# Kernel tuning notes

Measured on AMD Instinct MI355X. Metric: run time of the kernel, lower is better.

## Reference

```python
import jax, jax.numpy as jnp
import numpy as np

B, S, D, MAX_LEN = 4, 2048, 512, 2048
V = 2 * MAX_LEN + 1  # embedding table size
POS_MAX = 3000


def setup_inputs() -> dict:
    key = jax.random.key(0)
    k1, k2, k3 = jax.random.split(key, 3)
    x = jax.random.normal(k1, (B, S, D), dtype=jnp.float32)
    emb_table = jax.random.normal(k2, (V, D), dtype=jnp.float32) * 0.02
    positions = jnp.sort(jax.random.randint(k3, (B, S), 0, POS_MAX), axis=-1)
    return {"x": x, "emb_table": emb_table, "positions": positions}


def reference(x, emb_table, positions):
    # x: [B,S,D], emb_table: [2M+1, D], positions: [B,S] int
    Bc, Sc, _ = x.shape
    Vc = emb_table.shape[0]
    M = (Vc - 1) // 2
    # rel[b,i,j] = clamp(pos_i - pos_j, -M, M) + M   -> index into table
    rel = jnp.clip(positions[:, :, None] - positions[:, None, :], -M, M) + M  # [B,S,S]
    # mean_j emb[rel[b,i,j]] == (occurrence counts over V) @ table / S
    # counts[b,i,v] = #{j : rel[b,i,j] == v}; identical math, no [B,S,S,D] tensor.
    b_idx = jnp.arange(Bc)[:, None, None]
    i_idx = jnp.arange(Sc)[None, :, None]
    counts = jnp.zeros((Bc, Sc, Vc), dtype=x.dtype).at[b_idx, i_idx, rel].add(1.0)
    mean_emb = jnp.einsum('bsv,vd->bsd', counts, emb_table) / Sc  # [B,S,D]
    return x + mean_emb
```

## Files before the change

### kernel.cpp

```cpp
#include <hip/hip_runtime.h>
#include <hip/hip_bf16.h>
#include <cstdint>

#define NB 4
#define NS 2048
#define ND 512
#define NM 2048
#define NV 4097
#define NP 3000
#define TROW 8192
#define CCC 5104
#define EVW 4128
#define RSW 3080

typedef __bf16 bf16x8 __attribute__((ext_vector_type(8)));
typedef float f32x4 __attribute__((ext_vector_type(4)));

typedef const unsigned int __attribute__((address_space(1)))* as1_u32p;
typedef unsigned int __attribute__((address_space(3)))* as3_u32p;

__device__ __forceinline__ void gll16(const void* g, void* l) {
  __builtin_amdgcn_global_load_lds((as1_u32p)g, (as3_u32p)l, 16, 0, 0);
}

__device__ __forceinline__ unsigned short f2bf(float f) {
  union { __bf16 b; unsigned short u; } cv;
  cv.b = (__bf16)f;
  return cv.u;
}

__device__ __forceinline__ int lbound_dev(const int* a, int n, int key) {
  int lo = 0, hi = n;
  while (lo < hi) { int mid = (lo + hi) >> 1; if (a[mid] < key) lo = mid + 1; else hi = mid; }
  return lo;
}

__global__ void k1_hist(const int* __restrict__ pos, unsigned int* __restrict__ hist,
                        int* __restrict__ rs) {
  __shared__ unsigned int h[NP];
  int b = blockIdx.x, tid = threadIdx.x;
  for (int i = tid; i < NP; i += 256) h[i] = 0u;
  __syncthreads();
  const int* pb = pos + b * NS;
  for (int i = tid; i < NS; i += 256) atomicAdd(&h[pb[i]], 1u);
  __syncthreads();
  unsigned int* hb = hist + b * NP;
  for (int i = tid; i < NP; i += 256) hb[i] = h[i];
  for (int t = tid; t <= 3072; t += 256) rs[b * RSW + t] = lbound_dev(pb, NS, t);
}

__global__ void k2_htrev(const unsigned int* __restrict__ hist, unsigned short* __restrict__ HT) {
  int idx = blockIdx.x * 256 + threadIdx.x;
  int b = idx >> 14, rem = idx & 16383;
  int u = rem >> 10, t8 = rem & 1023;
  const unsigned int* hb = hist + b * NP;
  int basep = CCC + u - t8 * 8;
  union { unsigned short us[8]; uint4 v4; } pk;
#pragma unroll
  for (int e = 0; e < 8; ++e) {
    int p = basep - e;
    float f = (p >= 0 && p < NP) ? (float)hb[p] : 0.0f;
    pk.us[e] = f2bf(f);
  }
  *(uint4*)(HT + (size_t)(b * 16 + u) * TROW + t8 * 8) = pk.v4;
}

__global__ void k3_ebf(const float* __restrict__ emb, unsigned short* __restrict__ EB) {
  __shared__ float tile[64][65];
  int v0 = blockIdx.x * 64, d0 = blockIdx.y * 64, tid = threadIdx.x;
  int c = tid & 63, r0 = tid >> 6;
#pragma unroll
  for (int k = 0; k < 16; ++k) {
    int r = k * 4 + r0;
    int v = v0 + r;
    float val = 0.f;
    if (v < NV && v != 0 && v != (NV - 1)) val = emb[(size_t)v * ND + d0 + c];
    tile[r][c] = val;
  }
  __syncthreads();
  int vv0 = (tid & 7) * 8;
#pragma unroll
  for (int k2 = 0; k2 < 2; ++k2) {
    int dd = (tid >> 3) + k2 * 32;
    if (v0 + vv0 + 8 <= EVW) {
      union { unsigned short us[8]; uint4 v4; } pk;
#pragma unroll
      for (int e = 0; e < 8; ++e) pk.us[e] = f2bf(tile[vv0 + e][dd]);
      *(uint4*)(EB + (size_t)(d0 + dd) * EVW + v0 + vv0) = pk.v4;
    }
  }
}

__global__ __launch_bounds__(256, 3)
void k4_gemm(const unsigned short* __restrict__ HT, const unsigned short* __restrict__ EB,
             const int* __restrict__ rs, const float* __restrict__ x,
             const float* __restrict__ emb, float* __restrict__ out) {
  int Q0 = blockIdx.x * 64, d0 = blockIdx.y * 128, b = blockIdx.z;
  int tid = threadIdx.x, w = tid >> 6, lane = tid & 63;
  int wm = w >> 1, wn = w & 1;
  __shared__ unsigned short As[2][2048];
  __shared__ unsigned short Bs[2][4096];

  const unsigned short* HTb = HT + (size_t)b * 16 * TROW;
  int ul = lane & 15, gl = lane >> 4;

  int v_lo = (Q0 > 951) ? ((Q0 - 951) & ~31) : 0;
  int v_hi = Q0 + 2112; if (v_hi > EVW) v_hi = EVW;

  f32x4 acc[2][4];
#pragma unroll
  for (int a1 = 0; a1 < 2; ++a1)
#pragma unroll
    for (int a2 = 0; a2 < 4; ++a2) { f32x4 z = {0.f, 0.f, 0.f, 0.f}; acc[a1][a2] = z; }

  const unsigned short* asrc_lane = HTb + ul * TROW + gl * 8;

  auto stage = [&](int sbuf, int kk) {
    int t0 = CCC - Q0 - NM - 16 * w + kk;
    gll16(asrc_lane + t0, &As[sbuf][w * 512]);
#pragma unroll
    for (int ci = 0; ci < 2; ++ci) {
      int c = w + ci * 4;
      const unsigned short* bsrc = EB + (size_t)(d0 + c * 16 + ul) * EVW + kk + gl * 8;
      gll16(bsrc, &Bs[sbuf][c * 512]);
    }
  };

  stage(0, v_lo);
  __syncthreads();

  int aoff = (lane >> 4) * 128 + (lane & 15) * 8;
  int buf = 0;
  for (int kk = v_lo; kk < v_hi; kk += 32) {
    if (kk + 32 < v_hi) stage(buf ^ 1, kk + 32);
    bf16x8 af[2], bfr[4];
#pragma unroll
    for (int mf = 0; mf < 2; ++mf)
      af[mf] = *reinterpret_cast<const bf16x8*>(&As[buf][(wm * 2 + mf) * 512 + aoff]);
#pragma unroll
    for (int nf = 0; nf < 4; ++nf)
      bfr[nf] = *reinterpret_cast<const bf16x8*>(&Bs[buf][(wn * 4 + nf) * 512 + aoff]);
#pragma unroll
    for (int mf = 0; mf < 2; ++mf)
#pragma unroll
      for (int nf = 0; nf < 4; ++nf)
        acc[mf][nf] = __builtin_amdgcn_mfma_f32_16x16x32_bf16(af[mf], bfr[nf], acc[mf][nf], 0, 0, 0);
    __syncthreads();
    buf ^= 1;
  }

  const int* rsb = rs + b * RSW;
  const float* xb = x + (size_t)b * NS * ND;
  float* outb = out + (size_t)b * NS * ND;
  int col = lane & 15, rb4 = (lane >> 4) * 4;
#pragma unroll
  for (int nf = 0; nf < 4; ++nf) {
    int dcol = d0 + wn * 64 + nf * 16 + col;
    float e0v = emb[dcol];
    float eMv = emb[(size_t)(NV - 1) * ND + dcol];
#pragma unroll
    for (int mf = 0; mf < 2; ++mf) {
#pragma unroll
      for (int j = 0; j < 4; ++j) {
        int q = Q0 + wm * 32 + mf * 16 + rb4 + j;
        if (q >= NP) continue;
        int i0 = rsb[q], i1 = rsb[q + 1];
        if (i0 == i1) continue;
        int cge = (q >= NM) ? rsb[q - NM + 1] : 0;
        int cle = (q + NM < NP) ? (NS - rsb[q + NM]) : 0;
        float val = (acc[mf][nf][j] + (float)cge * eMv + (float)cle * e0v) * (1.0f / (float)NS);
        for (int i = i0; i < i1; ++i)
          outb[(size_t)i * ND + dcol] = xb[(size_t)i * ND + dcol] + val;
      }
    }
  }
}

extern "C" void kernel_launch(void* const* d_in, const int* in_sizes, int n_in,
                              void* d_out, int out_size, void* d_ws, size_t ws_size,
                              hipStream_t stream) {
  const float* x = (const float*)d_in[0];
  const float* emb = (const float*)d_in[1];
  const int* pos = (const int*)d_in[2];
  float* out = (float*)d_out;

  char* ws = (char*)d_ws;
  unsigned short* HT = (unsigned short*)(ws);
  unsigned short* EB = (unsigned short*)(ws + 1048576);
  unsigned int* hist = (unsigned int*)(ws + 5275648);
  int* rs = (int*)(ws + 5323648);

  hipLaunchKernelGGL(k1_hist, dim3(NB), dim3(256), 0, stream, pos, hist, rs);
  hipLaunchKernelGGL(k2_htrev, dim3(256), dim3(256), 0, stream, hist, HT);
  hipLaunchKernelGGL(k3_ebf, dim3(65, 8), dim3(256), 0, stream, emb, EB);
  hipLaunchKernelGGL(k4_gemm, dim3(47, 4, NB), dim3(256), 0, stream, HT, EB, rs, x, emb, out);
}
```

Before: 188.2 us.

## Triple-buffer GEMM LDS pipeline with manual waitcnt and split rank-search kernel

The GEMM main loop moves from double to triple buffering of the A/B LDS tiles. It uses explicit s_waitcnt vmcnt/lgkmcnt plus a single barrier per iteration, so async global-to-LDS loads run two tiles ahead, and it raises wave priority around the MFMA block. The binary-search rank computation leaves the 4-block histogram kernel for its own wider-grid kernel, so it gets more parallelism. Occupancy hint goes from 3 to 4 blocks per CU. The trade-offs are more LDS per block, an extra kernel launch, and hand-tuned waitcnt counts that must match the number of loads issued per stage.

```diff
diff --git a/kernel.cpp b/kernel.cpp
--- a/kernel.cpp
+++ b/kernel.cpp
@@ -35,8 +35,7 @@
   return lo;
 }
 
-__global__ void k1_hist(const int* __restrict__ pos, unsigned int* __restrict__ hist,
-                        int* __restrict__ rs) {
+__global__ void k1_hist(const int* __restrict__ pos, unsigned int* __restrict__ hist) {
   __shared__ unsigned int h[NP];
   int b = blockIdx.x, tid = threadIdx.x;
   for (int i = tid; i < NP; i += 256) h[i] = 0u;
@@ -46,7 +45,13 @@
   __syncthreads();
   unsigned int* hb = hist + b * NP;
   for (int i = tid; i < NP; i += 256) hb[i] = h[i];
-  for (int t = tid; t <= 3072; t += 256) rs[b * RSW + t] = lbound_dev(pb, NS, t);
+}
+
+__global__ void k1b_rs(const int* __restrict__ pos, int* __restrict__ rs) {
+  int t = blockIdx.x * 256 + threadIdx.x;
+  int b = blockIdx.y;
+  if (t > 3072) return;
+  rs[b * RSW + t] = lbound_dev(pos + b * NS, NS, t);
 }
 
 __global__ void k2_htrev(const unsigned int* __restrict__ hist, unsigned short* __restrict__ HT) {
@@ -91,21 +96,22 @@
   }
 }
 
-__global__ __launch_bounds__(256, 3)
+__global__ __launch_bounds__(256, 4)
 void k4_gemm(const unsigned short* __restrict__ HT, const unsigned short* __restrict__ EB,
              const int* __restrict__ rs, const float* __restrict__ x,
              const float* __restrict__ emb, float* __restrict__ out) {
   int Q0 = blockIdx.x * 64, d0 = blockIdx.y * 128, b = blockIdx.z;
   int tid = threadIdx.x, w = tid >> 6, lane = tid & 63;
   int wm = w >> 1, wn = w & 1;
-  __shared__ unsigned short As[2][2048];
-  __shared__ unsigned short Bs[2][4096];
+  __shared__ unsigned short As[3][2048];
+  __shared__ unsigned short Bs[3][4096];
 
   const unsigned short* HTb = HT + (size_t)b * 16 * TROW;
   int ul = lane & 15, gl = lane >> 4;
 
   int v_lo = (Q0 > 951) ? ((Q0 - 951) & ~31) : 0;
   int v_hi = Q0 + 2112; if (v_hi > EVW) v_hi = EVW;
+  int nt = (v_hi - v_lo) >> 5;
 
   f32x4 acc[2][4];
 #pragma unroll
@@ -115,7 +121,8 @@
 
   const unsigned short* asrc_lane = HTb + ul * TROW + gl * 8;
 
-  auto stage = [&](int sbuf, int kk) {
+  auto stage = [&](int sbuf, int t) {
+    int kk = v_lo + t * 32;
     int t0 = CCC - Q0 - NM - 16 * w + kk;
     gll16(asrc_lane + t0, &As[sbuf][w * 512]);
 #pragma unroll
@@ -126,27 +133,32 @@
     }
   };
 
-  stage(0, v_lo);
-  __syncthreads();
+  stage(0, 0);
+  stage(1, 1);
 
   int aoff = (lane >> 4) * 128 + (lane & 15) * 8;
-  int buf = 0;
-  for (int kk = v_lo; kk < v_hi; kk += 32) {
-    if (kk + 32 < v_hi) stage(buf ^ 1, kk + 32);
+  int s0 = 0, s1 = 1, s2 = 2;
+  for (int t = 0; t < nt; ++t) {
+    if (t + 1 < nt) asm volatile("s_waitcnt vmcnt(3) lgkmcnt(0)" ::: "memory");
+    else            asm volatile("s_waitcnt vmcnt(0) lgkmcnt(0)" ::: "memory");
+    __builtin_amdgcn_s_barrier();
+    if (t + 2 < nt) stage(s2, t + 2);
+
     bf16x8 af[2], bfr[4];
 #pragma unroll
     for (int mf = 0; mf < 2; ++mf)
-      af[mf] = *reinterpret_cast<const bf16x8*>(&As[buf][(wm * 2 + mf) * 512 + aoff]);
+      af[mf] = *reinterpret_cast<const bf16x8*>(&As[s0][(wm * 2 + mf) * 512 + aoff]);
 #pragma unroll
     for (int nf = 0; nf < 4; ++nf)
-      bfr[nf] = *reinterpret_cast<const bf16x8*>(&Bs[buf][(wn * 4 + nf) * 512 + aoff]);
+      bfr[nf] = *reinterpret_cast<const bf16x8*>(&Bs[s0][(wn * 4 + nf) * 512 + aoff]);
+    __builtin_amdgcn_s_setprio(1);
 #pragma unroll
     for (int mf = 0; mf < 2; ++mf)
 #pragma unroll
       for (int nf = 0; nf < 4; ++nf)
         acc[mf][nf] = __builtin_amdgcn_mfma_f32_16x16x32_bf16(af[mf], bfr[nf], acc[mf][nf], 0, 0, 0);
-    __syncthreads();
-    buf ^= 1;
+    __builtin_amdgcn_s_setprio(0);
+    int tmp = s0; s0 = s1; s1 = s2; s2 = tmp;
   }
 
   const int* rsb = rs + b * RSW;
@@ -190,7 +202,8 @@
   unsigned int* hist = (unsigned int*)(ws + 5275648);
   int* rs = (int*)(ws + 5323648);
 
-  hipLaunchKernelGGL(k1_hist, dim3(NB), dim3(256), 0, stream, pos, hist, rs);
+  hipLaunchKernelGGL(k1_hist, dim3(NB), dim3(256), 0, stream, pos, hist);
+  hipLaunchKernelGGL(k1b_rs, dim3(13, NB), dim3(256), 0, stream, pos, rs);
   hipLaunchKernelGGL(k2_htrev, dim3(256), dim3(256), 0, stream, hist, HT);
   hipLaunchKernelGGL(k3_ebf, dim3(65, 8), dim3(256), 0, stream, emb, EB);
   hipLaunchKernelGGL(k4_gemm, dim3(47, 4, NB), dim3(256), 0, stream, HT, EB, rs, x, emb, out);
```

Result: faster. 178.7 us (-5.1%).

## Pre-swizzle operands into MFMA fragment layout and drop LDS staging in GEMM

Applied to the files above, without the earlier changes.

The Toeplitz histogram and the bf16 embedding table are now written in a fragment-interleaved layout, so each lane loads its MFMA operand straight from global memory with one 16-byte load. The GEMM no longer stages through LDS or calls __syncthreads. Instead each wave owns a 32x64 tile with per-wave K bounds and keeps a three-deep register prefetch. The rank-search, Toeplitz build and embedding conversion kernels are merged into one prep launch, and the k1_hist work is split so rs is computed in parallel blocks. In exchange, operands are no longer shared between waves through LDS, which means more global and L2 traffic.

```diff
diff --git a/kernel.cpp b/kernel.cpp
--- a/kernel.cpp
+++ b/kernel.cpp
@@ -8,20 +8,12 @@
 #define NM 2048
 #define NV 4097
 #define NP 3000
-#define TROW 8192
-#define CCC 5104
-#define EVW 4128
 #define RSW 3080
+#define EBI_KB 129
+#define HTI_BATCH_BYTES (2 * 256 * 1024)
 
 typedef __bf16 bf16x8 __attribute__((ext_vector_type(8)));
 typedef float f32x4 __attribute__((ext_vector_type(4)));
-
-typedef const unsigned int __attribute__((address_space(1)))* as1_u32p;
-typedef unsigned int __attribute__((address_space(3)))* as3_u32p;
-
-__device__ __forceinline__ void gll16(const void* g, void* l) {
-  __builtin_amdgcn_global_load_lds((as1_u32p)g, (as3_u32p)l, 16, 0, 0);
-}
 
 __device__ __forceinline__ unsigned short f2bf(float f) {
   union { __bf16 b; unsigned short u; } cv;
@@ -35,8 +27,7 @@
   return lo;
 }
 
-__global__ void k1_hist(const int* __restrict__ pos, unsigned int* __restrict__ hist,
-                        int* __restrict__ rs) {
+__global__ void k1_hist(const int* __restrict__ pos, unsigned int* __restrict__ hist) {
   __shared__ unsigned int h[NP];
   int b = blockIdx.x, tid = threadIdx.x;
   for (int i = tid; i < NP; i += 256) h[i] = 0u;
@@ -46,66 +37,114 @@
   __syncthreads();
   unsigned int* hb = hist + b * NP;
   for (int i = tid; i < NP; i += 256) hb[i] = h[i];
-  for (int t = tid; t <= 3072; t += 256) rs[b * RSW + t] = lbound_dev(pb, NS, t);
-}
-
-__global__ void k2_htrev(const unsigned int* __restrict__ hist, unsigned short* __restrict__ HT) {
-  int idx = blockIdx.x * 256 + threadIdx.x;
-  int b = idx >> 14, rem = idx & 16383;
-  int u = rem >> 10, t8 = rem & 1023;
-  const unsigned int* hb = hist + b * NP;
-  int basep = CCC + u - t8 * 8;
-  union { unsigned short us[8]; uint4 v4; } pk;
-#pragma unroll
-  for (int e = 0; e < 8; ++e) {
-    int p = basep - e;
-    float f = (p >= 0 && p < NP) ? (float)hb[p] : 0.0f;
-    pk.us[e] = f2bf(f);
-  }
-  *(uint4*)(HT + (size_t)(b * 16 + u) * TROW + t8 * 8) = pk.v4;
-}
-
-__global__ void k3_ebf(const float* __restrict__ emb, unsigned short* __restrict__ EB) {
+}
+
+__global__ void k_prep(const int* __restrict__ pos, const unsigned int* __restrict__ hist,
+                       const float* __restrict__ emb, unsigned short* __restrict__ HTI,
+                       unsigned short* __restrict__ EBI, int* __restrict__ rs) {
   __shared__ float tile[64][65];
-  int v0 = blockIdx.x * 64, d0 = blockIdx.y * 64, tid = threadIdx.x;
-  int c = tid & 63, r0 = tid >> 6;
-#pragma unroll
-  for (int k = 0; k < 16; ++k) {
-    int r = k * 4 + r0;
-    int v = v0 + r;
-    float val = 0.f;
-    if (v < NV && v != 0 && v != (NV - 1)) val = emb[(size_t)v * ND + d0 + c];
-    tile[r][c] = val;
-  }
-  __syncthreads();
-  int vv0 = (tid & 7) * 8;
-#pragma unroll
-  for (int k2 = 0; k2 < 2; ++k2) {
-    int dd = (tid >> 3) + k2 * 32;
-    if (v0 + vv0 + 8 <= EVW) {
-      union { unsigned short us[8]; uint4 v4; } pk;
-#pragma unroll
-      for (int e = 0; e < 8; ++e) pk.us[e] = f2bf(tile[vv0 + e][dd]);
-      *(uint4*)(EB + (size_t)(d0 + dd) * EVW + v0 + vv0) = pk.v4;
-    }
-  }
-}
-
-__global__ __launch_bounds__(256, 3)
-void k4_gemm(const unsigned short* __restrict__ HT, const unsigned short* __restrict__ EB,
+  int blk = blockIdx.x, tid = threadIdx.x;
+  if (blk < 52) {
+    int b = blk & 3, chunk = blk >> 2;
+    int t = chunk * 256 + tid;
+    if (t <= 3072) rs[b * RSW + t] = lbound_dev(pos + b * NS, NS, t);
+    return;
+  }
+  if (blk < 564) {
+    int idx = (blk - 52) * 256 + tid;
+    int l = idx & 63;
+    int tb = (idx >> 6) & 255;
+    int p = (idx >> 14) & 1;
+    int bb = idx >> 15;
+    const unsigned int* hbt = hist + bb * NP;
+    int base = 5104 + (l & 15) - tb * 32 - p * 16 - ((l >> 4) * 8);
+    union { unsigned short us[8]; uint4 v4; } pk;
+#pragma unroll
+    for (int e = 0; e < 8; ++e) {
+      int ii = base - e;
+      float f = (ii >= 0 && ii < NP) ? (float)hbt[ii] : 0.0f;
+      pk.us[e] = f2bf(f);
+    }
+    *(uint4*)(HTI + ((size_t)(bb * 2 + p) * 256 + tb) * 512 + l * 8) = pk.v4;
+    return;
+  }
+  {
+    int blk2 = blk - 564;
+    int v0 = (blk2 % 65) * 64, d0 = (blk2 / 65) * 64;
+    int c = tid & 63, r0 = tid >> 6;
+#pragma unroll
+    for (int k = 0; k < 16; ++k) {
+      int r = k * 4 + r0;
+      int v = v0 + r;
+      float val = 0.f;
+      if (v < NV && v != 0 && v != (NV - 1)) val = emb[(size_t)v * ND + d0 + c];
+      tile[r][c] = val;
+    }
+    __syncthreads();
+#pragma unroll
+    for (int rep = 0; rep < 2; ++rep) {
+      int tile_id = rep * 4 + (tid >> 6);
+      int l = tid & 63;
+      int kb_loc = tile_id >> 2, dt_loc = tile_id & 3;
+      int kb = (v0 >> 5) + kb_loc, dt = (d0 >> 4) + dt_loc;
+      if (kb < EBI_KB) {
+        union { unsigned short us[8]; uint4 v4; } pk;
+#pragma unroll
+        for (int e = 0; e < 8; ++e)
+          pk.us[e] = f2bf(tile[kb_loc * 32 + ((l >> 4) * 8) + e][dt_loc * 16 + (l & 15)]);
+        *(uint4*)(EBI + ((size_t)dt * EBI_KB + kb) * 512 + l * 8) = pk.v4;
+      }
+    }
+  }
+}
+
+#define LOADSET(sa0, sa1, sb0, sb1, sb2, sb3, tt)                                   \
+  if ((tt) < nt) {                                                                  \
+    int tof = (tt) * 1024 + vo;                                                     \
+    sa0 = *(const bf16x8*)(hb + (size_t)(cA0 + tof));                               \
+    sa1 = *(const bf16x8*)(hb + (size_t)(cA1 + tof));                               \
+    sb0 = *(const bf16x8*)(eb + (size_t)(cB0 + tof));                               \
+    sb1 = *(const bf16x8*)(eb + (size_t)(cB1 + tof));                               \
+    sb2 = *(const bf16x8*)(eb + (size_t)(cB2 + tof));                               \
+    sb3 = *(const bf16x8*)(eb + (size_t)(cB3 + tof));                               \
+  }
+
+#define MMSET(sa0, sa1, sb0, sb1, sb2, sb3)                                         \
+  acc[0][0] = __builtin_amdgcn_mfma_f32_16x16x32_bf16(sa0, sb0, acc[0][0], 0, 0, 0);\
+  acc[0][1] = __builtin_amdgcn_mfma_f32_16x16x32_bf16(sa0, sb1, acc[0][1], 0, 0, 0);\
+  acc[0][2] = __builtin_amdgcn_mfma_f32_16x16x32_bf16(sa0, sb2, acc[0][2], 0, 0, 0);\
+  acc[0][3] = __builtin_amdgcn_mfma_f32_16x16x32_bf16(sa0, sb3, acc[0][3], 0, 0, 0);\
+  acc[1][0] = __builtin_amdgcn_mfma_f32_16x16x32_bf16(sa1, sb0, acc[1][0], 0, 0, 0);\
+  acc[1][1] = __builtin_amdgcn_mfma_f32_16x16x32_bf16(sa1, sb1, acc[1][1], 0, 0, 0);\
+  acc[1][2] = __builtin_amdgcn_mfma_f32_16x16x32_bf16(sa1, sb2, acc[1][2], 0, 0, 0);\
+  acc[1][3] = __builtin_amdgcn_mfma_f32_16x16x32_bf16(sa1, sb3, acc[1][3], 0, 0, 0);
+
+__global__ __launch_bounds__(256, 4)
+void k4_gemm(const unsigned short* __restrict__ HTI, const unsigned short* __restrict__ EBI,
              const int* __restrict__ rs, const float* __restrict__ x,
              const float* __restrict__ emb, float* __restrict__ out) {
-  int Q0 = blockIdx.x * 64, d0 = blockIdx.y * 128, b = blockIdx.z;
   int tid = threadIdx.x, w = tid >> 6, lane = tid & 63;
-  int wm = w >> 1, wn = w & 1;
-  __shared__ unsigned short As[2][2048];
-  __shared__ unsigned short Bs[2][4096];
-
-  const unsigned short* HTb = HT + (size_t)b * 16 * TROW;
-  int ul = lane & 15, gl = lane >> 4;
-
-  int v_lo = (Q0 > 951) ? ((Q0 - 951) & ~31) : 0;
-  int v_hi = Q0 + 2112; if (v_hi > EVW) v_hi = EVW;
+  int b = blockIdx.z;
+  int Q0w = blockIdx.x * 128 + w * 32;
+  int D0w = blockIdx.y * 64;
+
+  int v_lo = (Q0w > 951) ? ((Q0w - 951) & ~31) : 0;
+  int v_hi = Q0w + 2080; if (v_hi > 4128) v_hi = 4128;
+  int nt = (v_hi - v_lo) >> 5;
+
+  const char* hb = (const char*)HTI + (size_t)b * HTI_BATCH_BYTES;
+  const char* eb = (const char*)EBI;
+
+  int S0 = 3056 - Q0w + v_lo;
+  int S1 = S0 - 16;
+  int cA0 = (((S0 >> 4) & 1) * 256 + (S0 >> 5)) * 1024;
+  int cA1 = (((S1 >> 4) & 1) * 256 + (S1 >> 5)) * 1024;
+  int kb0 = v_lo >> 5, dt0 = D0w >> 4;
+  int cB0 = ((dt0 + 0) * EBI_KB + kb0) * 1024;
+  int cB1 = ((dt0 + 1) * EBI_KB + kb0) * 1024;
+  int cB2 = ((dt0 + 2) * EBI_KB + kb0) * 1024;
+  int cB3 = ((dt0 + 3) * EBI_KB + kb0) * 1024;
+  int vo = lane * 16;
 
   f32x4 acc[2][4];
 #pragma unroll
@@ -113,40 +152,24 @@
 #pragma unroll
     for (int a2 = 0; a2 < 4; ++a2) { f32x4 z = {0.f, 0.f, 0.f, 0.f}; acc[a1][a2] = z; }
 
-  const unsigned short* asrc_lane = HTb + ul * TROW + gl * 8;
-
-  auto stage = [&](int sbuf, int kk) {
-    int t0 = CCC - Q0 - NM - 16 * w + kk;
-    gll16(asrc_lane + t0, &As[sbuf][w * 512]);
-#pragma unroll
-    for (int ci = 0; ci < 2; ++ci) {
-      int c = w + ci * 4;
-      const unsigned short* bsrc = EB + (size_t)(d0 + c * 16 + ul) * EVW + kk + gl * 8;
-      gll16(bsrc, &Bs[sbuf][c * 512]);
-    }
-  };
-
-  stage(0, v_lo);
-  __syncthreads();
-
-  int aoff = (lane >> 4) * 128 + (lane & 15) * 8;
-  int buf = 0;
-  for (int kk = v_lo; kk < v_hi; kk += 32) {
-    if (kk + 32 < v_hi) stage(buf ^ 1, kk + 32);
-    bf16x8 af[2], bfr[4];
-#pragma unroll
-    for (int mf = 0; mf < 2; ++mf)
-      af[mf] = *reinterpret_cast<const bf16x8*>(&As[buf][(wm * 2 + mf) * 512 + aoff]);
-#pragma unroll
-    for (int nf = 0; nf < 4; ++nf)
-      bfr[nf] = *reinterpret_cast<const bf16x8*>(&Bs[buf][(wn * 4 + nf) * 512 + aoff]);
-#pragma unroll
-    for (int mf = 0; mf < 2; ++mf)
-#pragma unroll
-      for (int nf = 0; nf < 4; ++nf)
-        acc[mf][nf] = __builtin_amdgcn_mfma_f32_16x16x32_bf16(af[mf], bfr[nf], acc[mf][nf], 0, 0, 0);
-    __syncthreads();
-    buf ^= 1;
+  bf16x8 a00, a01, b00, b01, b02, b03;
+  bf16x8 a10, a11, b10, b11, b12, b13;
+  bf16x8 a20, a21, b20, b21, b22, b23;
+
+  LOADSET(a00, a01, b00, b01, b02, b03, 0);
+  LOADSET(a10, a11, b10, b11, b12, b13, 1);
+
+  int t = 0;
+  for (;;) {
+    LOADSET(a20, a21, b20, b21, b22, b23, t + 2);
+    MMSET(a00, a01, b00, b01, b02, b03);
+    if (++t == nt) break;
+    LOADSET(a00, a01, b00, b01, b02, b03, t + 2);
+    MMSET(a10, a11, b10, b11, b12, b13);
+    if (++t == nt) break;
+    LOADSET(a10, a11, b10, b11, b12, b13, t + 2);
+    MMSET(a20, a21, b20, b21, b22, b23);
+    if (++t == nt) break;
   }
 
   const int* rsb = rs + b * RSW;
@@ -155,14 +178,14 @@
   int col = lane & 15, rb4 = (lane >> 4) * 4;
 #pragma unroll
   for (int nf = 0; nf < 4; ++nf) {
-    int dcol = d0 + wn * 64 + nf * 16 + col;
+    int dcol = D0w + nf * 16 + col;
     float e0v = emb[dcol];
     float eMv = emb[(size_t)(NV - 1) * ND + dcol];
 #pragma unroll
     for (int mf = 0; mf < 2; ++mf) {
 #pragma unroll
       for (int j = 0; j < 4; ++j) {
-        int q = Q0 + wm * 32 + mf * 16 + rb4 + j;
+        int q = Q0w + mf * 16 + rb4 + j;
         if (q >= NP) continue;
         int i0 = rsb[q], i1 = rsb[q + 1];
         if (i0 == i1) continue;
@@ -185,13 +208,12 @@
   float* out = (float*)d_out;
 
   char* ws = (char*)d_ws;
-  unsigned short* HT = (unsigned short*)(ws);
-  unsigned short* EB = (unsigned short*)(ws + 1048576);
-  unsigned int* hist = (unsigned int*)(ws + 5275648);
-  int* rs = (int*)(ws + 5323648);
-
-  hipLaunchKernelGGL(k1_hist, dim3(NB), dim3(256), 0, stream, pos, hist, rs);
-  hipLaunchKernelGGL(k2_htrev, dim3(256), dim3(256), 0, stream, hist, HT);
-  hipLaunchKernelGGL(k3_ebf, dim3(65, 8), dim3(256), 0, stream, emb, EB);
-  hipLaunchKernelGGL(k4_gemm, dim3(47, 4, NB), dim3(256), 0, stream, HT, EB, rs, x, emb, out);
-}
+  unsigned short* HTI = (unsigned short*)(ws);
+  unsigned short* EBI = (unsigned short*)(ws + 2097152);
+  unsigned int* hist = (unsigned int*)(ws + 6324224);
+  int* rs = (int*)(ws + 6372224);
+
+  hipLaunchKernelGGL(k1_hist, dim3(NB), dim3(256), 0, stream, pos, hist);
+  hipLaunchKernelGGL(k_prep, dim3(1084), dim3(256), 0, stream, pos, hist, emb, HTI, EBI, rs);
+  hipLaunchKernelGGL(k4_gemm, dim3(24, 8, NB), dim3(256), 0, stream, HTI, EBI, rs, x, emb, out);
+}
```

Result: faster. 159.8 us (-15.1%).
